# Optimization experiments

Hardware: AMD Instinct MI355X
Metric: run time of the kernel (lower is better)

Reference implementation:

```python
import jax, jax.numpy as jnp
import numpy as np

B, T, IMG, PATCH = 4, 16, 256, 16
G = IMG // PATCH            # 16
P = G * G                   # 256 patches
PP = PATCH * PATCH          # 256 pixels per patch
H, FF, L, NH = 512, 2048, 4, 8
MASK_BIAS = 20.0
SKIP_PAIRS = [(0, 2), (0, 3), (1, 3), (0, 4), (1, 4), (2, 4)]


def _ln(x, g, b):
    m = x.mean(-1, keepdims=True)
    v = ((x - m) ** 2).mean(-1, keepdims=True)
    return (x - m) * jax.lax.rsqrt(v + 1e-5) * g + b


def _attn(x, wq, bq, wk, bk, wv, bv, wo, wo_mask, mask):
    # x: (B, G, S, D) -- attention over axis S within each (B, G) group
    Bx, Gx, S, D = x.shape
    hd = D // NH
    scale = hd ** -0.5

    def proj(w, b_):
        y = jnp.einsum('bgsd,ed->bgse', x, w) + b_
        return y.reshape(Bx, Gx, S, NH, hd).transpose(0, 1, 3, 2, 4)  # (B,G,NH,S,hd)

    q, k, v = proj(wq, bq), proj(wk, bk), proj(wv, bv)
    scores = jnp.einsum('bgnsh,bgnth->bgnst', q, k) * scale + (mask - 0.5) * MASK_BIAS
    a = jax.nn.softmax(scores, axis=-1)
    o = jnp.einsum('bgnst,bgnth->bgnsh', a, v).transpose(0, 1, 3, 2, 4).reshape(Bx, Gx, S, D)
    return jnp.einsum('bgsd,ed->bgse', o, wo * wo_mask)  # masked W_o, no bias


def _forward(x, s_mask, t_mask, wo_masks, ff_masks, skip_masks, head_mask,
             patch_w, patch_b, temporal_pos, spatial_pos,
             sq_w, sq_b, sk_w, sk_b, sv_w, sv_b, so_w,
             tq_w, tq_b, tk_w, tk_b, tv_w, tv_b, to_w,
             ln_s_g, ln_s_b, ln_t_g, ln_t_b, ln_f_g, ln_f_b,
             ff1_w, ff1_b, ff2_w, ff2_b, skip_w, lnf_g, lnf_b, head_w, head_b):
    Bx = x.shape[0]
    # patch embed: (B,T,IMG,IMG) -> (B,T,P,PP) -> (B,T,P,H)
    xp = x.reshape(Bx, T, G, PATCH, G, PATCH).transpose(0, 1, 2, 4, 3, 5).reshape(Bx, T, P, PP)
    tokens = jnp.einsum('btpq,hq->btph', xp, patch_w) + patch_b
    tokens = tokens + temporal_pos + spatial_pos

    acts = [tokens]
    for i in range(L):
        h = acts[i]
        wm = wo_masks[i]
        # spatial attention over P within each frame
        s_out = _attn(_ln(h, ln_s_g[i], ln_s_b[i]),
                      sq_w[i], sq_b[i], sk_w[i], sk_b[i], sv_w[i], sv_b[i],
                      so_w[i], wm, s_mask)
        h = h + s_out
        # temporal attention over T at each patch position
        ht = _ln(h, ln_t_g[i], ln_t_b[i]).transpose(0, 2, 1, 3)  # (B,P,T,H)
        t_out = _attn(ht, tq_w[i], tq_b[i], tk_w[i], tk_b[i], tv_w[i], tv_b[i],
                      to_w[i], wm, t_mask).transpose(0, 2, 1, 3)
        h = h + t_out
        # masked FFN
        hf = _ln(h, ln_f_g[i], ln_f_b[i])
        f1 = jax.nn.relu(jnp.einsum('btpd,fd->btpf', hf, ff1_w[i] * ff_masks[i]) + ff1_b[i])
        h = h + jnp.einsum('btpf,df->btpd', f1, ff2_w[i]) + ff2_b[i]
        # cross-layer masked skip connections into layer i+1
        for si, (src, tgt) in enumerate(SKIP_PAIRS):
            if tgt != i + 1:
                continue
            h = h + jnp.einsum('btpd,ed->btpe', acts[src], skip_w[si] * skip_masks[si])
        acts.append(h)

    final = _ln(acts[-1], lnf_g, lnf_b)
    last = final[:, -1]  # (B,P,H) last frame
    patches = jax.nn.sigmoid(jnp.einsum('bpd,qd->bpq', last, head_w * head_mask) + head_b)
    pred = patches.reshape(Bx, G, G, PATCH, PATCH).transpose(0, 1, 3, 2, 4).reshape(Bx, IMG, IMG)
    return pred


def setup_inputs() -> dict:
    key = jax.random.key(0)
    ks = iter(jax.random.split(key, 64))
    nrm = lambda sh: jax.random.normal(next(ks), sh, dtype=jnp.float32) * 0.02
    uni = lambda sh: jax.random.uniform(next(ks), sh, dtype=jnp.float32)
    d = {}
    d['x'] = jax.random.normal(next(ks), (B, T, IMG, IMG), dtype=jnp.float32)
    d['s_mask'] = uni((P, P))
    d['t_mask'] = uni((T, T))
    d['wo_masks'] = uni((L, H, H))
    d['ff_masks'] = uni((L, FF, H))
    d['skip_masks'] = uni((len(SKIP_PAIRS), H, H))
    d['head_mask'] = uni((PP, H))
    d['patch_w'] = nrm((H, PP)); d['patch_b'] = jnp.zeros((H,), jnp.float32)
    d['temporal_pos'] = nrm((1, T, 1, H))
    d['spatial_pos'] = nrm((1, 1, P, H))
    for pre in ['sq', 'sk', 'sv', 'tq', 'tk', 'tv']:
        d[pre + '_w'] = nrm((L, H, H)); d[pre + '_b'] = jnp.zeros((L, H), jnp.float32)
    d['so_w'] = nrm((L, H, H)); d['to_w'] = nrm((L, H, H))
    for pre in ['ln_s', 'ln_t', 'ln_f']:
        d[pre + '_g'] = jnp.ones((L, H), jnp.float32); d[pre + '_b'] = jnp.zeros((L, H), jnp.float32)
    d['ff1_w'] = nrm((L, FF, H)); d['ff1_b'] = jnp.zeros((L, FF), jnp.float32)
    d['ff2_w'] = nrm((L, H, FF)); d['ff2_b'] = jnp.zeros((L, H), jnp.float32)
    d['skip_w'] = nrm((len(SKIP_PAIRS), H, H))
    d['lnf_g'] = jnp.ones((H,), jnp.float32); d['lnf_b'] = jnp.zeros((H,), jnp.float32)
    d['head_w'] = nrm((PP, H)); d['head_b'] = jnp.zeros((PP,), jnp.float32)
    return d


def reference(x, s_mask, t_mask, wo_masks, ff_masks, skip_masks, head_mask,
              patch_w, patch_b, temporal_pos, spatial_pos,
              sq_w, sq_b, sk_w, sk_b, sv_w, sv_b, so_w,
              tq_w, tq_b, tk_w, tk_b, tv_w, tv_b, to_w,
              ln_s_g, ln_s_b, ln_t_g, ln_t_b, ln_f_g, ln_f_b,
              ff1_w, ff1_b, ff2_w, ff2_b, skip_w, lnf_g, lnf_b, head_w, head_b):
    return _forward(x, s_mask, t_mask, wo_masks, ff_masks, skip_masks, head_mask,
                    patch_w, patch_b, temporal_pos, spatial_pos,
                    sq_w, sq_b, sk_w, sk_b, sv_w, sv_b, so_w,
                    tq_w, tq_b, tk_w, tk_b, tv_w, tv_b, to_w,
                    ln_s_g, ln_s_b, ln_t_g, ln_t_b, ln_f_g, ln_f_b,
                    ff1_w, ff1_b, ff2_w, ff2_b, skip_w, lnf_g, lnf_b, head_w, head_b)
```

## Files before the change

kernel.cpp:

```cpp
#include <hip/hip_runtime.h>
#include <hip/hip_bf16.h>
#include <math.h>

#define BB 4
#define TT 16
#define IMGSZ 256
#define PPATCH 256
#define PQ 256
#define HH 512
#define FFDIM 2048
#define LLAYERS 4
#define NHEADS 8
#define HD 64

#define NTOK (BB*TT*PPATCH)

typedef unsigned short bfu;
typedef unsigned int u32;
typedef short bf16x8 __attribute__((ext_vector_type(8)));
typedef float f32x4 __attribute__((ext_vector_type(4)));

__device__ inline float bf2f(bfu u) {
    union { unsigned int i; float f; } cv; cv.i = ((unsigned int)u) << 16; return cv.f;
}
__device__ inline bfu f2bf(float f) {
    __hip_bfloat16 h = __float2bfloat16(f);
    union { __hip_bfloat16 h; bfu u; } cv; cv.h = h; return cv.u;
}
__device__ inline float u_lo(unsigned int u) {
    union { unsigned int i; float f; } cv; cv.i = u << 16; return cv.f;
}
__device__ inline float u_hi(unsigned int u) {
    union { unsigned int i; float f; } cv; cv.i = u & 0xffff0000u; return cv.f;
}
__device__ inline unsigned int pack2(float a, float b) {
    return (unsigned int)f2bf(a) | ((unsigned int)f2bf(b) << 16);
}
__device__ __forceinline__ void gload16(const void* g, void* l) {
    __builtin_amdgcn_global_load_lds(
        (const __attribute__((address_space(1))) u32*)g,
        (__attribute__((address_space(3))) u32*)l, 16, 0, 0);
}

#define WL_SQKV 0
#define WL_SO   786432
#define WL_TQKV 1048576
#define WL_TO   1835008
#define WL_FF1  2097152
#define WL_FF2  3145728
#define WL_TOT  4194304
#define WP_SKIP 0
#define WP_HEAD 1572864
#define WP_PATCH 1703936
#define WP_TOT  1835008

__global__ __launch_bounds__(256) void patchify_k(const float* __restrict__ x,
                                                  bfu* __restrict__ xp) {
    int idx = blockIdx.x * 256 + threadIdx.x;
    int col = idx & 255;
    int row = idx >> 8;
    int p   = row & 255;
    int bt  = row >> 8;
    int gr = p >> 4, gc = p & 15;
    int pr = col >> 4, pc = col & 15;
    xp[idx] = f2bf(x[(size_t)bt * 65536 + (gr * 16 + pr) * 256 + gc * 16 + pc]);
}

__global__ __launch_bounds__(256) void addpos_k(bfu* __restrict__ tok,
                                                const float* __restrict__ tpos,
                                                const float* __restrict__ spos) {
    int idx = blockIdx.x * 256 + threadIdx.x;
    int h = idx & 511;
    int p = (idx >> 9) & 255;
    int t = (idx >> 17) & 15;
    tok[idx] = f2bf(bf2f(tok[idx]) + tpos[t * HH + h] + spos[p * HH + h]);
}

__global__ __launch_bounds__(256) void convpers_k(const float* __restrict__ skw,
                                                  const float* __restrict__ skm,
                                                  const float* __restrict__ hw,
                                                  const float* __restrict__ hm,
                                                  const float* __restrict__ pw,
                                                  bfu* __restrict__ out) {
    int g8 = blockIdx.x * 256 + threadIdx.x;
    int idx = g8 * 8;
    const float* src; const float* msk = nullptr; int off;
    if (idx < WP_HEAD)       { src = skw; msk = skm; off = idx; }
    else if (idx < WP_PATCH) { src = hw;  msk = hm;  off = idx - WP_HEAD; }
    else                     { src = pw;             off = idx - WP_PATCH; }
    float4 a = *(const float4*)(src + off);
    float4 b = *(const float4*)(src + off + 4);
    if (msk) {
        float4 ma = *(const float4*)(msk + off), mb = *(const float4*)(msk + off + 4);
        a.x *= ma.x; a.y *= ma.y; a.z *= ma.z; a.w *= ma.w;
        b.x *= mb.x; b.y *= mb.y; b.z *= mb.z; b.w *= mb.w;
    }
    uint4 o = { pack2(a.x, a.y), pack2(a.z, a.w), pack2(b.x, b.y), pack2(b.z, b.w) };
    *(uint4*)(out + idx) = o;
}

__global__ __launch_bounds__(256) void convw_k(const float* __restrict__ sq, const float* __restrict__ sk,
                                               const float* __restrict__ sv, const float* __restrict__ so,
                                               const float* __restrict__ tq, const float* __restrict__ tk,
                                               const float* __restrict__ tv, const float* __restrict__ to,
                                               const float* __restrict__ ff1, const float* __restrict__ ff2,
                                               const float* __restrict__ wom, const float* __restrict__ ffm,
                                               const float* __restrict__ sqb, const float* __restrict__ skb,
                                               const float* __restrict__ svb, const float* __restrict__ tqb,
                                               const float* __restrict__ tkb, const float* __restrict__ tvb,
                                               bfu* __restrict__ out,
                                               float* __restrict__ bias_s, float* __restrict__ bias_t) {
    int g8 = blockIdx.x * 256 + threadIdx.x;
    if (g8 < 384) {
        int bi = g8 * 8;
        const float* bsrc; float* bdst;
        if (bi < 1536) {
            int o = bi; bdst = bias_s + o;
            bsrc = (o < 512 ? sqb : o < 1024 ? skb : svb) + (o & 511);
        } else {
            int o = bi - 1536; bdst = bias_t + o;
            bsrc = (o < 512 ? tqb : o < 1024 ? tkb : tvb) + (o & 511);
        }
        *(float4*)bdst = *(const float4*)bsrc;
        *(float4*)(bdst + 4) = *(const float4*)(bsrc + 4);
    }
    int idx = g8 * 8;
    const float* src; const float* msk = nullptr; int off;
    if (idx < WL_SO) {
        int r = idx; src = (r < 262144 ? sq : r < 524288 ? sk : sv); off = r & 262143;
    } else if (idx < WL_TQKV) { src = so; msk = wom; off = idx - WL_SO; }
    else if (idx < WL_TO) {
        int r = idx - WL_TQKV; src = (r < 262144 ? tq : r < 524288 ? tk : tv); off = r & 262143;
    } else if (idx < WL_FF1) { src = to; msk = wom; off = idx - WL_TO; }
    else if (idx < WL_FF2)   { src = ff1; msk = ffm; off = idx - WL_FF1; }
    else                     { src = ff2; off = idx - WL_FF2; }
    float4 a = *(const float4*)(src + off);
    float4 b = *(const float4*)(src + off + 4);
    if (msk) {
        float4 ma = *(const float4*)(msk + off), mb = *(const float4*)(msk + off + 4);
        a.x *= ma.x; a.y *= ma.y; a.z *= ma.z; a.w *= ma.w;
        b.x *= mb.x; b.y *= mb.y; b.z *= mb.z; b.w *= mb.w;
    }
    uint4 o = { pack2(a.x, a.y), pack2(a.z, a.w), pack2(b.x, b.y), pack2(b.z, b.w) };
    *(uint4*)(out + idx) = o;
}

__global__ __launch_bounds__(256) void ln_k(const bfu* __restrict__ X,
                                            const float* __restrict__ g,
                                            const float* __restrict__ b,
                                            bfu* __restrict__ Y,
                                            int rows, int mode) {
    int wave = threadIdx.x >> 6;
    int lane = threadIdx.x & 63;
    int row = blockIdx.x * 4 + wave;
    if (row >= rows) return;
    int inRow = row, outRow = row;
    if (mode == 2) {
        int bb = row >> 8; int p = row & 255;
        inRow = ((bb * TT + (TT - 1)) << 8) + p;
    } else if (mode == 1) {
        int bb = row >> 12;
        int r  = row & 4095;
        int t  = r >> 8;
        int p  = r & 255;
        outRow = (((bb << 8) + p) << 4) + t;
    }
    const bfu* xr = X + (size_t)inRow * HH;
    bfu vv[8];
    *(uint4*)vv = *(const uint4*)(xr + lane * 8);
    float v[8];
    float s = 0.f;
    #pragma unroll
    for (int i = 0; i < 8; i++) { v[i] = bf2f(vv[i]); s += v[i]; }
    #pragma unroll
    for (int off = 32; off; off >>= 1) s += __shfl_xor(s, off, 64);
    float mean = s * (1.f / 512.f);
    float vs = 0.f;
    #pragma unroll
    for (int i = 0; i < 8; i++) { float d = v[i] - mean; vs += d * d; }
    #pragma unroll
    for (int off = 32; off; off >>= 1) vs += __shfl_xor(vs, off, 64);
    float rstd = rsqrtf(vs * (1.f / 512.f) + 1e-5f);
    bfu out[8];
    #pragma unroll
    for (int i = 0; i < 8; i++) {
        int c = lane * 8 + i;
        out[i] = f2bf((v[i] - mean) * rstd * g[c] + b[c]);
    }
    *(uint4*)(Y + (size_t)outRow * HH + lane * 8) = *(uint4*)out;
}

__device__ __forceinline__ void seg_ptrs(int s,
    const bfu* A0, const bfu* W0, int K0, const bfu* A1, const bfu* W1, int K1,
    const bfu* A2, const bfu* W2, int K2, const bfu* A3, const bfu* W3, int K3,
    const bfu*& pa, const bfu*& pw, int& kk) {
    switch (s) {
        case 0:  pa = A0; pw = W0; kk = K0; break;
        case 1:  pa = A1; pw = W1; kk = K1; break;
        case 2:  pa = A2; pw = W2; kk = K2; break;
        default: pa = A3; pw = W3; kk = K3; break;
    }
}

template<int ACT>
__global__ __launch_bounds__(256) void gemm3_k(
    const bfu* __restrict__ A0, const bfu* __restrict__ W0, int K0,
    const bfu* __restrict__ A1, const bfu* __restrict__ W1, int K1,
    const bfu* __restrict__ A2, const bfu* __restrict__ W2, int K2,
    const bfu* __restrict__ A3, const bfu* __restrict__ W3, int K3,
    int nseg,
    const float* __restrict__ bias, const bfu* __restrict__ addTo,
    bfu* __restrict__ C, int M, int N, int nx) {
    __shared__ __align__(16) bfu As[2][128 * 32];
    __shared__ __align__(16) bfu Bs[2][128 * 32];
    const int nwg = gridDim.x;
    const int id = blockIdx.x;
    const int q = nwg >> 3, r = nwg & 7;
    const int xcd = id & 7, sub = id >> 3;
    const int wid = (xcd < r ? xcd * (q + 1) : r * (q + 1) + (xcd - r) * q) + sub;
    const int bm = (wid / nx) * 128, bn = (wid % nx) * 128;

    const int tid = threadIdx.x, wave = tid >> 6, lane = tid & 63;
    const int wr = (wave >> 1) * 64, wc = (wave & 1) * 64;
    const int srow = wave * 32 + (lane >> 2);
    const int skoff = (lane & 3) * 8;
    const int frow = lane & 15, fk = (lane >> 4) * 8;

    const bfu *pa, *pw; int kseg;
    int seg = 0;
    seg_ptrs(0, A0, W0, K0, A1, W1, K1, A2, W2, K2, A3, W3, K3, pa, pw, kseg);
    const bfu* as0 = pa + (size_t)(bm + srow) * kseg + skoff;
    const bfu* as1 = as0 + (size_t)16 * kseg;
    const bfu* ws0 = pw + (size_t)(bn + srow) * kseg + skoff;
    const bfu* ws1 = ws0 + (size_t)16 * kseg;
    int kleft = kseg;
    const int tot = (K0 + K1 + K2 + K3) >> 5;

    f32x4 acc[4][4];
    const f32x4 zero = {0.f, 0.f, 0.f, 0.f};
    #pragma unroll
    for (int m = 0; m < 4; m++)
        #pragma unroll
        for (int n = 0; n < 4; n++) acc[m][n] = zero;

    #define STAGE(buf)                                                         \
        do {                                                                   \
            gload16(as0, &As[buf][(wave * 32) * 32]);                          \
            gload16(as1, &As[buf][(wave * 32 + 16) * 32]);                     \
            gload16(ws0, &Bs[buf][(wave * 32) * 32]);                          \
            gload16(ws1, &Bs[buf][(wave * 32 + 16) * 32]);                     \
            as0 += 32; as1 += 32; ws0 += 32; ws1 += 32;                        \
            kleft -= 32;                                                       \
            if (kleft == 0 && seg + 1 < nseg) {                                \
                seg++;                                                         \
                seg_ptrs(seg, A0, W0, K0, A1, W1, K1, A2, W2, K2, A3, W3, K3,  \
                         pa, pw, kseg);                                        \
                as0 = pa + (size_t)(bm + srow) * kseg + skoff;                 \
                as1 = as0 + (size_t)16 * kseg;                                 \
                ws0 = pw + (size_t)(bn + srow) * kseg + skoff;                 \
                ws1 = ws0 + (size_t)16 * kseg;                                 \
                kleft = kseg;                                                  \
            }                                                                  \
        } while (0)

    #define COMPUTE(buf)                                                       \
        do {                                                                   \
            bf16x8 af[4], bfr[4];                                              \
            _Pragma("unroll")                                                  \
            for (int m = 0; m < 4; m++)                                        \
                af[m] = *(const bf16x8*)&As[buf][(wr + m * 16 + frow) * 32 + fk]; \
            _Pragma("unroll")                                                  \
            for (int n = 0; n < 4; n++)                                        \
                bfr[n] = *(const bf16x8*)&Bs[buf][(wc + n * 16 + frow) * 32 + fk]; \
            _Pragma("unroll")                                                  \
            for (int m = 0; m < 4; m++)                                        \
                _Pragma("unroll")                                              \
                for (int n = 0; n < 4; n++)                                    \
                    acc[m][n] = __builtin_amdgcn_mfma_f32_16x16x32_bf16(       \
                        af[m], bfr[n], acc[m][n], 0, 0, 0);                    \
        } while (0)

    STAGE(0);
    __syncthreads();
    int cur = 0;
    for (int t = 0; t < tot - 1; t++) {
        STAGE(cur ^ 1);
        COMPUTE(cur);
        __syncthreads();
        cur ^= 1;
    }
    COMPUTE(cur);
    #undef STAGE
    #undef COMPUTE

    const int erow = (lane >> 4) * 4, ecol = lane & 15;
    #pragma unroll
    for (int m = 0; m < 4; m++) {
        #pragma unroll
        for (int n = 0; n < 4; n++) {
            int gcol = bn + wc + n * 16 + ecol;
            float bsv = bias ? bias[gcol] : 0.f;
            #pragma unroll
            for (int r2 = 0; r2 < 4; r2++) {
                int grow = bm + wr + m * 16 + erow + r2;
                float v = acc[m][n][r2] + bsv;
                if (ACT == 1) v = v > 0.f ? v : 0.f;
                if (ACT == 2) v = 1.f / (1.f + __expf(-v));
                if (addTo) v += bf2f(addTo[(size_t)grow * N + gcol]);
                C[(size_t)grow * N + gcol] = f2bf(v);
            }
        }
    }
}

#define VTS 264
#define PTS 72
__global__ __launch_bounds__(256, 2) void sattn_k(const bfu* __restrict__ QKV,
                                                  const float* __restrict__ mask,
                                                  bfu* __restrict__ O) {
    __shared__ __align__(16) bfu Vt[64][VTS];
    __shared__ __align__(16) bfu Pt[4][64][PTS];
    const int gh = blockIdx.x, g = gh >> 3, head = gh & 7;
    const int tid = threadIdx.x, wave = tid >> 6, lane = tid & 63;
    const size_t rbase = (size_t)g * 256;
    const size_t qoff = (size_t)head * 64, koff = qoff + 512, voff = qoff + 1024;

    {
        const bfu* vp = QKV + (rbase + tid) * 1536 + voff;
        bfu vals[64];
        #pragma unroll
        for (int c = 0; c < 8; c++) *(uint4*)&vals[c * 8] = *(const uint4*)(vp + c * 8);
        #pragma unroll
        for (int d = 0; d < 64; d++) Vt[d][tid] = vals[d];
    }
    __syncthreads();

    const int l15 = lane & 15, l4 = lane >> 4;
    const int wq0 = wave * 64;

    bf16x8 Qb[4][2];
    #pragma unroll
    for (int n = 0; n < 4; n++)
        #pragma unroll
        for (int kr = 0; kr < 2; kr++)
            Qb[n][kr] = *(const bf16x8*)(QKV + (rbase + wq0 + n * 16 + l15) * 1536 + qoff + kr * 32 + l4 * 8);

    f32x4 acc_o[4][4];
    const f32x4 zero = {0.f, 0.f, 0.f, 0.f};
    #pragma unroll
    for (int m = 0; m < 4; m++)
        #pragma unroll
        for (int n = 0; n < 4; n++) acc_o[m][n] = zero;
    float m_run[4] = {-3e38f, -3e38f, -3e38f, -3e38f};
    float l_run[4] = {0.f, 0.f, 0.f, 0.f};

    for (int kt = 0; kt < 4; kt++) {
        f32x4 acc_s[4][4];
        #pragma unroll
        for (int m = 0; m < 4; m++)
            #pragma unroll
            for (int n = 0; n < 4; n++) acc_s[m][n] = zero;
        #pragma unroll
        for (int m = 0; m < 4; m++) {
            const bfu* kp = QKV + (rbase + kt * 64 + m * 16 + l15) * 1536 + koff + l4 * 8;
            bf16x8 Ka0 = *(const bf16x8*)kp;
            bf16x8 Ka1 = *(const bf16x8*)(kp + 32);
            #pragma unroll
            for (int n = 0; n < 4; n++) {
                acc_s[m][n] = __builtin_amdgcn_mfma_f32_16x16x32_bf16(Ka0, Qb[n][0], acc_s[m][n], 0, 0, 0);
                acc_s[m][n] = __builtin_amdgcn_mfma_f32_16x16x32_bf16(Ka1, Qb[n][1], acc_s[m][n], 0, 0, 0);
            }
        }
        #pragma unroll
        for (int m = 0; m < 4; m++)
            #pragma unroll
            for (int n = 0; n < 4; n++) {
                float4 mv = *(const float4*)(mask + (size_t)(wq0 + n * 16 + l15) * 256 + kt * 64 + m * 16 + l4 * 4);
                acc_s[m][n][0] = acc_s[m][n][0] * 0.125f + (mv.x - 0.5f) * 20.f;
                acc_s[m][n][1] = acc_s[m][n][1] * 0.125f + (mv.y - 0.5f) * 20.f;
                acc_s[m][n][2] = acc_s[m][n][2] * 0.125f + (mv.z - 0.5f) * 20.f;
                acc_s[m][n][3] = acc_s[m][n][3] * 0.125f + (mv.w - 0.5f) * 20.f;
            }
        #pragma unroll
        for (int n = 0; n < 4; n++) {
            float tmax = acc_s[0][n][0];
            #pragma unroll
            for (int m = 0; m < 4; m++)
                #pragma unroll
                for (int r = 0; r < 4; r++) tmax = fmaxf(tmax, acc_s[m][n][r]);
            tmax = fmaxf(tmax, __shfl_xor(tmax, 16, 64));
            tmax = fmaxf(tmax, __shfl_xor(tmax, 32, 64));
            float newm = fmaxf(m_run[n], tmax);
            float corr = __expf(m_run[n] - newm);
            m_run[n] = newm;
            float esum = 0.f;
            #pragma unroll
            for (int m = 0; m < 4; m++) {
                #pragma unroll
                for (int r = 0; r < 4; r++) {
                    float p = __expf(acc_s[m][n][r] - newm);
                    acc_s[m][n][r] = p;
                    esum += p;
                }
            }
            esum += __shfl_xor(esum, 16, 64);
            esum += __shfl_xor(esum, 32, 64);
            l_run[n] = l_run[n] * corr + esum;
            #pragma unroll
            for (int m = 0; m < 4; m++) {
                acc_o[m][n][0] *= corr; acc_o[m][n][1] *= corr;
                acc_o[m][n][2] *= corr; acc_o[m][n][3] *= corr;
            }
            #pragma unroll
            for (int m = 0; m < 4; m++) {
                uint2 pw = { pack2(acc_s[m][n][0], acc_s[m][n][1]),
                             pack2(acc_s[m][n][2], acc_s[m][n][3]) };
                *(uint2*)&Pt[wave][n * 16 + l15][m * 16 + l4 * 4] = pw;
            }
        }
        #pragma unroll
        for (int kr = 0; kr < 2; kr++) {
            bf16x8 Va[4], Pb[4];
            #pragma unroll
            for (int m = 0; m < 4; m++)
                Va[m] = *(const bf16x8*)&Vt[m * 16 + l15][kt * 64 + kr * 32 + l4 * 8];
            #pragma unroll
            for (int n = 0; n < 4; n++)
                Pb[n] = *(const bf16x8*)&Pt[wave][n * 16 + l15][kr * 32 + l4 * 8];
            #pragma unroll
            for (int m = 0; m < 4; m++)
                #pragma unroll
                for (int n = 0; n < 4; n++)
                    acc_o[m][n] = __builtin_amdgcn_mfma_f32_16x16x32_bf16(Va[m], Pb[n], acc_o[m][n], 0, 0, 0);
        }
    }

    float inv[4];
    #pragma unroll
    for (int n = 0; n < 4; n++) inv[n] = 1.f / l_run[n];
    #pragma unroll
    for (int m = 0; m < 4; m++)
        #pragma unroll
        for (int n = 0; n < 4; n++) {
            ushort4 ov = { f2bf(acc_o[m][n][0] * inv[n]), f2bf(acc_o[m][n][1] * inv[n]),
                           f2bf(acc_o[m][n][2] * inv[n]), f2bf(acc_o[m][n][3] * inv[n]) };
            *(ushort4*)(O + (rbase + wq0 + n * 16 + l15) * 512 + head * 64 + m * 16 + l4 * 4) = ov;
        }
}

__global__ __launch_bounds__(256) void tattn_k(const bfu* __restrict__ QKV,
                                               const float* __restrict__ mask,
                                               bfu* __restrict__ O) {
    __shared__ __align__(16) bfu Ks[16][520];
    __shared__ __align__(16) bfu Vs[16][520];
    __shared__ __align__(16) bfu Qs[16][520];
    const int bp = blockIdx.x, b = bp >> 8, p = bp & 255;
    const int tid = threadIdx.x, wave = tid >> 6, lane = tid & 63;
    const size_t rb = (size_t)bp * 16;
    {
        int r = tid >> 4, off = (tid & 15) * 32;
        const bfu* qp = QKV + (rb + r) * 1536 + off;
        const bfu* kp = qp + 512;
        const bfu* vp = qp + 1024;
        #pragma unroll
        for (int c = 0; c < 32; c += 8) {
            *(uint4*)&Qs[r][off + c] = *(const uint4*)(qp + c);
            *(uint4*)&Ks[r][off + c] = *(const uint4*)(kp + c);
            *(uint4*)&Vs[r][off + c] = *(const uint4*)(vp + c);
        }
    }
    __syncthreads();
    const int qq = lane >> 4, kk = lane & 15;
    const int dp4 = (lane & 15) * 4;
    const int abase = lane & 48;
    for (int hh = 0; hh < 2; hh++) {
        const int head = wave * 2 + hh, hoff = head * 64;
        for (int qp4 = 0; qp4 < 4; qp4++) {
            const int q = qp4 * 4 + qq;
            float dot = 0.f;
            #pragma unroll
            for (int dg = 0; dg < 8; dg++) {
                const unsigned int* kp = (const unsigned int*)&Ks[kk][hoff + dg * 8];
                const unsigned int* qp = (const unsigned int*)&Qs[q][hoff + dg * 8];
                #pragma unroll
                for (int c = 0; c < 4; c++) {
                    unsigned int ku = kp[c], qu = qp[c];
                    dot += u_lo(ku) * u_lo(qu) + u_hi(ku) * u_hi(qu);
                }
            }
            float sc = dot * 0.125f + (mask[q * 16 + kk] - 0.5f) * 20.f;
            float m = sc;
            #pragma unroll
            for (int off = 1; off < 16; off <<= 1) m = fmaxf(m, __shfl_xor(m, off, 64));
            float e = __expf(sc - m);
            float sum = e;
            #pragma unroll
            for (int off = 1; off < 16; off <<= 1) sum += __shfl_xor(sum, off, 64);
            float a = e / sum;
            float o0 = 0.f, o1 = 0.f, o2 = 0.f, o3 = 0.f;
            #pragma unroll
            for (int k = 0; k < 16; k++) {
                float ak = __shfl(a, abase + k, 64);
                const unsigned int* vp = (const unsigned int*)&Vs[k][hoff + dp4];
                unsigned int u0 = vp[0], u1 = vp[1];
                o0 += ak * u_lo(u0); o1 += ak * u_hi(u0);
                o2 += ak * u_lo(u1); o3 += ak * u_hi(u1);
            }
            size_t orow = ((size_t)((b * 16 + q) * 256 + p)) * 512 + hoff + dp4;
            ushort4 ov = { f2bf(o0), f2bf(o1), f2bf(o2), f2bf(o3) };
            *(ushort4*)(O + orow) = ov;
        }
    }
}

__global__ __launch_bounds__(256) void unpatch_k(const bfu* __restrict__ patches,
                                                 float* __restrict__ pred) {
    int idx = blockIdx.x * 256 + threadIdx.x;
    int c = idx & 255;
    int r = (idx >> 8) & 255;
    int bb = idx >> 16;
    int gr = r >> 4, pr = r & 15, gc = c >> 4, pc = c & 15;
    pred[idx] = bf2f(patches[((size_t)(bb * 256 + gr * 16 + gc) << 8) + pr * 16 + pc]);
}

static inline void run_gseg(int act,
                            const bfu* A0, const bfu* W0, int K0,
                            const bfu* A1, const bfu* W1, int K1,
                            const bfu* A2, const bfu* W2, int K2,
                            const bfu* A3, const bfu* W3, int K3, int nseg,
                            const float* bias, const bfu* addTo, bfu* C,
                            int M, int N, hipStream_t s) {
    int nx = N / 128;
    int nwg = nx * (M / 128);
    if (act == 0)
        gemm3_k<0><<<nwg, 256, 0, s>>>(A0, W0, K0, A1, W1, K1, A2, W2, K2, A3, W3, K3,
                                       nseg, bias, addTo, C, M, N, nx);
    else if (act == 1)
        gemm3_k<1><<<nwg, 256, 0, s>>>(A0, W0, K0, A1, W1, K1, A2, W2, K2, A3, W3, K3,
                                       nseg, bias, addTo, C, M, N, nx);
    else
        gemm3_k<2><<<nwg, 256, 0, s>>>(A0, W0, K0, A1, W1, K1, A2, W2, K2, A3, W3, K3,
                                       nseg, bias, addTo, C, M, N, nx);
}

static inline void run_g(int act, const bfu* A, const bfu* W, int K,
                         const float* bias, const bfu* addTo, bfu* C,
                         int M, int N, hipStream_t s) {
    run_gseg(act, A, W, K, nullptr, nullptr, 0, nullptr, nullptr, 0,
             nullptr, nullptr, 0, 1, bias, addTo, C, M, N, s);
}

extern "C" void kernel_launch(void* const* d_in, const int* in_sizes, int n_in,
                              void* d_out, int out_size, void* d_ws, size_t ws_size,
                              hipStream_t stream) {
    const float* x        = (const float*)d_in[0];
    const float* s_mask   = (const float*)d_in[1];
    const float* t_mask   = (const float*)d_in[2];
    const float* wo_masks = (const float*)d_in[3];
    const float* ff_masks = (const float*)d_in[4];
    const float* skip_masks = (const float*)d_in[5];
    const float* head_mask  = (const float*)d_in[6];
    const float* patch_w  = (const float*)d_in[7];
    const float* patch_b  = (const float*)d_in[8];
    const float* tpos     = (const float*)d_in[9];
    const float* spos     = (const float*)d_in[10];
    const float* sq_w = (const float*)d_in[11];
    const float* sq_b = (const float*)d_in[12];
    const float* sk_w = (const float*)d_in[13];
    const float* sk_b = (const float*)d_in[14];
    const float* sv_w = (const float*)d_in[15];
    const float* sv_b = (const float*)d_in[16];
    const float* tq_w = (const float*)d_in[17];
    const float* tq_b = (const float*)d_in[18];
    const float* tk_w = (const float*)d_in[19];
    const float* tk_b = (const float*)d_in[20];
    const float* tv_w = (const float*)d_in[21];
    const float* tv_b = (const float*)d_in[22];
    const float* so_w = (const float*)d_in[23];
    const float* to_w = (const float*)d_in[24];
    const float* ln_s_g = (const float*)d_in[25];
    const float* ln_s_b = (const float*)d_in[26];
    const float* ln_t_g = (const float*)d_in[27];
    const float* ln_t_b = (const float*)d_in[28];
    const float* ln_f_g = (const float*)d_in[29];
    const float* ln_f_b = (const float*)d_in[30];
    const float* ff1_w = (const float*)d_in[31];
    const float* ff1_b = (const float*)d_in[32];
    const float* ff2_w = (const float*)d_in[33];
    const float* ff2_b = (const float*)d_in[34];
    const float* skip_w = (const float*)d_in[35];
    const float* lnf_g = (const float*)d_in[36];
    const float* lnf_b = (const float*)d_in[37];
    const float* head_w = (const float*)d_in[38];
    const float* head_b = (const float*)d_in[39];

    bfu* ws = (bfu*)d_ws;
    const size_t ACTE = (size_t)NTOK * HH;
    bfu* acts[5];
    for (int i = 0; i < 5; i++) acts[i] = ws + i * ACTE;
    bfu* xln = ws + 5 * ACTE;
    bfu* qkv = ws + 6 * ACTE;
    bfu* ob  = ws + 9 * ACTE;
    bfu* f1  = qkv;
    bfu* xp      = ob;
    bfu* lastln  = xln;
    bfu* patches = qkv;
    bfu* wlayer = ws + 10 * ACTE;
    bfu* wpers  = wlayer + WL_TOT;
    float* bias_s = (float*)(wpers + WP_TOT);
    float* bias_t = bias_s + 1536;

    convpers_k<<<WP_TOT / 8 / 256, 256, 0, stream>>>(skip_w, skip_masks, head_w, head_mask,
                                                     patch_w, wpers);

    patchify_k<<<NTOK * PQ / 256, 256, 0, stream>>>(x, xp);
    run_g(0, xp, wpers + WP_PATCH, PQ, patch_b, nullptr, acts[0], NTOK, HH, stream);
    addpos_k<<<NTOK * HH / 256, 256, 0, stream>>>(acts[0], tpos, spos);

    const size_t WS = 512 * 512;
    const size_t FS = 2048 * 512;
    const int srcs[6] = {0, 0, 1, 0, 1, 2};
    const int tgts[6] = {2, 3, 3, 4, 4, 4};

    for (int i = 0; i < LLAYERS; i++) {
        bfu* h   = acts[i];
        bfu* hn  = acts[i + 1];
        convw_k<<<WL_TOT / 8 / 256, 256, 0, stream>>>(
            sq_w + i * WS, sk_w + i * WS, sv_w + i * WS, so_w + i * WS,
            tq_w + i * WS, tk_w + i * WS, tv_w + i * WS, to_w + i * WS,
            ff1_w + i * FS, ff2_w + i * FS,
            wo_masks + i * WS, ff_masks + i * FS,
            sq_b + i * HH, sk_b + i * HH, sv_b + i * HH,
            tq_b + i * HH, tk_b + i * HH, tv_b + i * HH,
            wlayer, bias_s, bias_t);
        ln_k<<<NTOK / 4, 256, 0, stream>>>(h, ln_s_g + i * HH, ln_s_b + i * HH, xln, NTOK, 0);
        run_g(0, xln, wlayer + WL_SQKV, HH, bias_s, nullptr, qkv, NTOK, 1536, stream);
        sattn_k<<<BB * TT * NHEADS, 256, 0, stream>>>(qkv, s_mask, ob);
        run_g(0, ob, wlayer + WL_SO, HH, nullptr, h, hn, NTOK, HH, stream);
        ln_k<<<NTOK / 4, 256, 0, stream>>>(hn, ln_t_g + i * HH, ln_t_b + i * HH, xln, NTOK, 1);
        run_g(0, xln, wlayer + WL_TQKV, HH, bias_t, nullptr, qkv, NTOK, 1536, stream);
        tattn_k<<<BB * PPATCH, 256, 0, stream>>>(qkv, t_mask, ob);
        run_g(0, ob, wlayer + WL_TO, HH, nullptr, hn, hn, NTOK, HH, stream);
        ln_k<<<NTOK / 4, 256, 0, stream>>>(hn, ln_f_g + i * HH, ln_f_b + i * HH, xln, NTOK, 0);
        run_g(1, xln, wlayer + WL_FF1, HH, ff1_b + i * FFDIM, nullptr, f1, NTOK, FFDIM, stream);
        {
            const bfu* Aseg[4] = { f1, nullptr, nullptr, nullptr };
            const bfu* Wseg[4] = { wlayer + WL_FF2, nullptr, nullptr, nullptr };
            int Kseg[4] = { FFDIM, 0, 0, 0 };
            int ns = 1;
            for (int si = 0; si < 6; si++) {
                if (tgts[si] != i + 1) continue;
                Aseg[ns] = acts[srcs[si]];
                Wseg[ns] = wpers + WP_SKIP + si * WS;
                Kseg[ns] = HH;
                ns++;
            }
            run_gseg(0, Aseg[0], Wseg[0], Kseg[0], Aseg[1], Wseg[1], Kseg[1],
                     Aseg[2], Wseg[2], Kseg[2], Aseg[3], Wseg[3], Kseg[3], ns,
                     ff2_b + i * HH, hn, hn, NTOK, HH, stream);
        }
    }

    ln_k<<<(BB * PPATCH) / 4, 256, 0, stream>>>(acts[4], lnf_g, lnf_b, lastln, BB * PPATCH, 2);
    run_g(2, lastln, wpers + WP_HEAD, HH, head_b, nullptr, patches, BB * PPATCH, PQ, stream);
    unpatch_k<<<BB * IMGSZ * IMGSZ / 256, 256, 0, stream>>>(patches, (float*)d_out);
}
```

Measured before the change: 1.509 ms.

## Triple-buffer GEMM shared tiles with vmcnt waits and swizzle LDS layout

The bf16 MFMA GEMM moves from double to triple buffering in shared memory, so two tiles stay in flight. The __syncthreads calls are replaced with explicit s_waitcnt vmcnt(4)/vmcnt(0) plus s_barrier, so only the oldest stage's loads are waited on. The k-offset used for storing and reading tiles is also XOR-swizzled to cut LDS bank conflicts on the fragment reads. This adds shared memory (48KB per block), which may lower occupancy. It also relies on the vmcnt counts matching the four direct-to-LDS loads issued per stage.

New measurement: 1.468 ms. 2.7% less time.

```diff
diff --git a/kernel.cpp b/kernel.cpp
--- a/kernel.cpp
+++ b/kernel.cpp
@@ -211,8 +211,7 @@
     int nseg,
     const float* __restrict__ bias, const bfu* __restrict__ addTo,
     bfu* __restrict__ C, int M, int N, int nx) {
-    __shared__ __align__(16) bfu As[2][128 * 32];
-    __shared__ __align__(16) bfu Bs[2][128 * 32];
+    __shared__ __align__(16) bfu S[3][2][128 * 32];
     const int nwg = gridDim.x;
     const int id = blockIdx.x;
     const int q = nwg >> 3, r = nwg & 7;
@@ -223,8 +222,9 @@
     const int tid = threadIdx.x, wave = tid >> 6, lane = tid & 63;
     const int wr = (wave >> 1) * 64, wc = (wave & 1) * 64;
     const int srow = wave * 32 + (lane >> 2);
-    const int skoff = (lane & 3) * 8;
-    const int frow = lane & 15, fk = (lane >> 4) * 8;
+    const int skoff = (((lane & 3) ^ ((lane >> 3) & 3)) * 8);
+    const int frow = lane & 15;
+    const int fk = (((lane >> 4) ^ ((frow >> 1) & 3)) * 8);
 
     const bfu *pa, *pw; int kseg;
     int seg = 0;
@@ -245,10 +245,10 @@
 
     #define STAGE(buf)                                                         \
         do {                                                                   \
-            gload16(as0, &As[buf][(wave * 32) * 32]);                          \
-            gload16(as1, &As[buf][(wave * 32 + 16) * 32]);                     \
-            gload16(ws0, &Bs[buf][(wave * 32) * 32]);                          \
-            gload16(ws1, &Bs[buf][(wave * 32 + 16) * 32]);                     \
+            gload16(as0, &S[buf][0][(wave * 32) * 32]);                        \
+            gload16(as1, &S[buf][0][(wave * 32 + 16) * 32]);                   \
+            gload16(ws0, &S[buf][1][(wave * 32) * 32]);                        \
+            gload16(ws1, &S[buf][1][(wave * 32 + 16) * 32]);                   \
             as0 += 32; as1 += 32; ws0 += 32; ws1 += 32;                        \
             kleft -= 32;                                                       \
             if (kleft == 0 && seg + 1 < nseg) {                                \
@@ -268,10 +268,10 @@
             bf16x8 af[4], bfr[4];                                              \
             _Pragma("unroll")                                                  \
             for (int m = 0; m < 4; m++)                                        \
-                af[m] = *(const bf16x8*)&As[buf][(wr + m * 16 + frow) * 32 + fk]; \
+                af[m] = *(const bf16x8*)&S[buf][0][(wr + m * 16 + frow) * 32 + fk]; \
             _Pragma("unroll")                                                  \
             for (int n = 0; n < 4; n++)                                        \
-                bfr[n] = *(const bf16x8*)&Bs[buf][(wc + n * 16 + frow) * 32 + fk]; \
+                bfr[n] = *(const bf16x8*)&S[buf][1][(wc + n * 16 + frow) * 32 + fk]; \
             _Pragma("unroll")                                                  \
             for (int m = 0; m < 4; m++)                                        \
                 _Pragma("unroll")                                              \
@@ -280,18 +280,33 @@
                         af[m], bfr[n], acc[m][n], 0, 0, 0);                    \
         } while (0)
 
+    #define VWAIT4 do { asm volatile("s_waitcnt vmcnt(4)" ::: "memory");       \
+                        __builtin_amdgcn_sched_barrier(0); } while (0)
+    #define VWAIT0 do { asm volatile("s_waitcnt vmcnt(0)" ::: "memory");       \
+                        __builtin_amdgcn_sched_barrier(0); } while (0)
+    #define BAR    do { __builtin_amdgcn_s_barrier();                          \
+                        __builtin_amdgcn_sched_barrier(0); } while (0)
+
     STAGE(0);
-    __syncthreads();
-    int cur = 0;
-    for (int t = 0; t < tot - 1; t++) {
-        STAGE(cur ^ 1);
+    STAGE(1);
+    VWAIT4;
+    BAR;
+    int cur = 0, sb = 2;
+    for (int t = 0; t < tot; t++) {
+        const bool pf = (t + 2 < tot);
+        if (pf) { STAGE(sb); sb = (sb == 2) ? 0 : sb + 1; }
         COMPUTE(cur);
-        __syncthreads();
-        cur ^= 1;
-    }
-    COMPUTE(cur);
+        cur = (cur == 2) ? 0 : cur + 1;
+        if (t + 1 < tot) {
+            if (pf) { VWAIT4; } else { VWAIT0; }
+            BAR;
+        }
+    }
     #undef STAGE
     #undef COMPUTE
+    #undef VWAIT4
+    #undef VWAIT0
+    #undef BAR
 
     const int erow = (lane >> 4) * 4, ecol = lane & 15;
     #pragma unroll
```
